# Kernel optimization log

Measured on AMD Instinct MI355X. Metric: run time of the kernel, lower is better.

The kernel has to match this reference:

```python
import jax, jax.numpy as jnp
import numpy as np

N_USER = 50000
N_ITEM = 100000
N_NODES = N_USER + N_ITEM  # 150000
EMB = 64
N_LAYERS = 3
NNZ = 2400000
BATCH = 4096
EPS = 1e-12  # F.normalize eps


def setup_inputs() -> dict:
    key = jax.random.key(0)
    ks = jax.random.split(key, 12)
    return {
        "users": jax.random.randint(ks[0], (BATCH,), 0, N_USER, dtype=jnp.int32),
        "pos_items": jax.random.randint(ks[1], (BATCH,), 0, N_ITEM, dtype=jnp.int32),
        "neg_items": jax.random.randint(ks[2], (BATCH,), 0, N_ITEM, dtype=jnp.int32),
        "adj_row": jax.random.randint(ks[3], (NNZ,), 0, N_NODES, dtype=jnp.int32),
        "adj_col": jax.random.randint(ks[4], (NNZ,), 0, N_NODES, dtype=jnp.int32),
        "adj_val": jax.random.uniform(ks[5], (NNZ,), dtype=jnp.float32),
        "user_emb": jax.random.normal(ks[6], (N_USER, EMB), dtype=jnp.float32) * 0.1,
        "item_emb": jax.random.normal(ks[7], (N_ITEM, EMB), dtype=jnp.float32) * 0.1,
        "W_gc": jax.random.normal(ks[8], (N_LAYERS, EMB, EMB), dtype=jnp.float32) * 0.1,
        "b_gc": jax.random.normal(ks[9], (N_LAYERS, 1, EMB), dtype=jnp.float32) * 0.1,
        "W_bi": jax.random.normal(ks[10], (N_LAYERS, EMB, EMB), dtype=jnp.float32) * 0.1,
        "b_bi": jax.random.normal(ks[11], (N_LAYERS, 1, EMB), dtype=jnp.float32) * 0.1,
    }


def reference(users, pos_items, neg_items, adj_row, adj_col, adj_val,
              user_emb, item_emb, W_gc, b_gc, W_bi, b_bi):
    # ego embeddings: concat user/item tables -> [N_NODES, EMB]
    ego = jnp.concatenate([user_emb, item_emb], axis=0)
    all_embs = [ego]
    for k in range(N_LAYERS):
        # sparse A_hat @ ego via gather + segment-sum over edges
        msgs = adj_val[:, None] * ego[adj_col]            # [NNZ, EMB]
        side = jax.ops.segment_sum(msgs, adj_row, num_segments=N_NODES)
        sum_emb = side @ W_gc[k] + b_gc[k]                # [N, EMB]
        bi_emb = (ego * side) @ W_bi[k] + b_bi[k]         # [N, EMB]
        ego = jax.nn.leaky_relu(sum_emb + bi_emb, negative_slope=0.2)
        # mess_dropout = 0 (eval mode) -> identity
        nrm = jnp.linalg.norm(ego, axis=1, keepdims=True)
        all_embs.append(ego / jnp.maximum(nrm, EPS))
    all_embs = jnp.concatenate(all_embs, axis=1)          # [N, EMB*(L+1)]
    u_g = all_embs[:N_USER]
    i_g = all_embs[N_USER:]
    return (u_g[users], i_g[pos_items], i_g[neg_items])
```

## Files before the change

### kernel.cpp

```cpp
#include <hip/hip_runtime.h>

typedef short bf16x8 __attribute__((ext_vector_type(8)));
typedef float f32x4  __attribute__((ext_vector_type(4)));

#define N_USER 50000
#define N_ITEM 100000
#define N_NODES 150000
#define EMB 64
#define NNZ 2400000
#define BATCH 4096
#define NSAMP (3 * BATCH)
#define NB 256
#define RPB 587
#define BS_GRID 256
#define EPB (NNZ / BS_GRID)
#define CAP 10304

__device__ __forceinline__ unsigned int bf16_rne(float x) {
    unsigned int u = __float_as_uint(x);
    return (u + 0x7fffu + ((u >> 16) & 1u)) >> 16;
}
__device__ __forceinline__ float bflo(unsigned int u) { return __uint_as_float(u << 16); }
__device__ __forceinline__ float bfhi(unsigned int u) { return __uint_as_float(u & 0xffff0000u); }

__device__ __forceinline__ void fma8(float v, const uint4& x, float* acc) {
    acc[0] = fmaf(v, bflo(x.x), acc[0]); acc[1] = fmaf(v, bfhi(x.x), acc[1]);
    acc[2] = fmaf(v, bflo(x.y), acc[2]); acc[3] = fmaf(v, bfhi(x.y), acc[3]);
    acc[4] = fmaf(v, bflo(x.z), acc[4]); acc[5] = fmaf(v, bfhi(x.z), acc[5]);
    acc[6] = fmaf(v, bflo(x.w), acc[6]); acc[7] = fmaf(v, bfhi(x.w), acc[7]);
}
__device__ __forceinline__ uint4 pack8(const float* f) {
    return make_uint4((bf16_rne(f[1]) << 16) | bf16_rne(f[0]),
                      (bf16_rne(f[3]) << 16) | bf16_rne(f[2]),
                      (bf16_rne(f[5]) << 16) | bf16_rne(f[4]),
                      (bf16_rne(f[7]) << 16) | bf16_rne(f[6]));
}
__device__ __forceinline__ uint2 cvt2(const float4& v) {
    return make_uint2((bf16_rne(v.y) << 16) | bf16_rne(v.x),
                      (bf16_rne(v.w) << 16) | bf16_rne(v.z));
}

#define SEG_A (N_NODES * 4)
#define SEG_B (NSAMP * 16)
#define SEG_C (3 * 8192)
#define SEG_D 192
#define INIT_TOT (SEG_A + SEG_B + SEG_C + SEG_D + NSAMP)
#define INIT_BLOCKS ((INIT_TOT + 1023) / 1024)
__global__ __launch_bounds__(1024) void binit(const float4* __restrict__ ue4,
                                              const float4* __restrict__ ie4,
                                              const int* __restrict__ users,
                                              const int* __restrict__ pos,
                                              const int* __restrict__ neg,
                                              uint2* __restrict__ ego_bf,
                                              float* __restrict__ out,
                                              int* __restrict__ samp,
                                              const float* __restrict__ Wgc,
                                              const float* __restrict__ Wbi,
                                              const float* __restrict__ bgc,
                                              const float* __restrict__ bbi,
                                              ushort* __restrict__ wbf,
                                              float* __restrict__ biasf) {
    int idx = blockIdx.x * 1024 + threadIdx.x;
    if (idx >= INIT_TOT) return;
    if (idx < SEG_A) {
        const int NU4 = N_USER * 16;
        int b4 = idx * 4;
        float4 a, b, c, d;
        if (b4 < NU4) { a = ue4[b4]; b = ue4[b4 + 1]; c = ue4[b4 + 2]; d = ue4[b4 + 3]; }
        else { int j = b4 - NU4; a = ie4[j]; b = ie4[j + 1]; c = ie4[j + 2]; d = ie4[j + 3]; }
        uint2 o0 = cvt2(a), o1 = cvt2(b), o2 = cvt2(c), o3 = cvt2(d);
        uint4* e4 = (uint4*)ego_bf;
        e4[idx * 2]     = make_uint4(o0.x, o0.y, o1.x, o1.y);
        e4[idx * 2 + 1] = make_uint4(o2.x, o2.y, o3.x, o3.y);
    } else if (idx < SEG_A + SEG_B) {
        int tt = idx - SEG_A;
        int r = tt >> 4, dq = tt & 15;
        int seg = r >> 12, bi = r & (BATCH - 1);
        int node = (seg == 0) ? users[bi] : N_USER + ((seg == 1) ? pos[bi] : neg[bi]);
        float4 v = (node < N_USER) ? ue4[node * 16 + dq] : ie4[(node - N_USER) * 16 + dq];
        ((float4*)out)[(size_t)r * 64 + dq] = v;
    } else if (idx < SEG_A + SEG_B + SEG_C) {
        int tt = idx - SEG_A - SEG_B;
        int l = tt >> 13, rem = tt & 8191;
        int k = rem >> 6, n = rem & 63;
        float w = (k < 64) ? Wgc[l * 4096 + k * 64 + n] : Wbi[l * 4096 + (k - 64) * 64 + n];
        wbf[l * 8704 + n * 136 + k] = (ushort)bf16_rne(w);
    } else if (idx < SEG_A + SEG_B + SEG_C + SEG_D) {
        int tt = idx - SEG_A - SEG_B - SEG_C;
        biasf[tt] = bgc[tt] + bbi[tt];
    } else {
        int tt = idx - SEG_A - SEG_B - SEG_C - SEG_D;
        int seg = tt >> 12, bi = tt & (BATCH - 1);
        samp[tt] = (seg == 0) ? users[bi] : N_USER + ((seg == 1) ? pos[bi] : neg[bi]);
    }
}

__global__ __launch_bounds__(1024) void bin_scatter(const int* __restrict__ rows,
                                                    const int* __restrict__ cols,
                                                    const float* __restrict__ vals,
                                                    int* __restrict__ gcur,
                                                    int2* __restrict__ tmp_cv) {
    __shared__ int2 sorted[EPB];
    __shared__ int hist[NB];
    __shared__ int excl[NB];
    __shared__ int cur[NB];
    __shared__ int gb[NB];
    const int t = threadIdx.x, blk = blockIdx.x;
    if (t < NB) { hist[t] = 0; cur[t] = 0; }
    __syncthreads();
    const int e0 = blk * EPB;
    for (int i = t; i < EPB; i += 1024) atomicAdd(&hist[rows[e0 + i] / RPB], 1);
    __syncthreads();
    if (t < NB) gb[t] = atomicAdd(&gcur[t], hist[t]);
    if (t < NB) excl[t] = hist[t];
    for (int off = 1; off < NB; off <<= 1) {
        __syncthreads();
        int add = (t < NB && t >= off) ? excl[t - off] : 0;
        __syncthreads();
        if (t < NB) excl[t] += add;
    }
    __syncthreads();
    for (int i = t; i < EPB; i += 1024) {
        int e = e0 + i;
        int r = rows[e];
        int b = r / RPB;
        int slot = atomicAdd(&cur[b], 1);
        unsigned vv = (__float_as_uint(vals[e]) & ~1023u) | (unsigned)(r - b * RPB);
        sorted[excl[b] - hist[b] + slot] = make_int2(cols[e], (int)vv);
    }
    __syncthreads();
    const int w = t >> 6, lane = t & 63;
    for (int b = w; b < NB; b += 16) {
        int lo = excl[b] - hist[b];
        int n = hist[b];
        int2* dst = tmp_cv + (size_t)b * CAP + gb[b];
        for (int k = lane; k < n; k += 64) dst[k] = sorted[lo + k];
    }
}

__global__ __launch_bounds__(1024) void csr_from_bins(const int* __restrict__ gcur,
                                                      const int2* __restrict__ tmp_cv,
                                                      int2* __restrict__ ecv,
                                                      int2* __restrict__ row_se) {
    __shared__ int rcnt[RPB];
    __shared__ int sc[1024];
    const int b = blockIdx.x;
    const int row0 = b * RPB;
    const int t = threadIdx.x;
    const int beg = b * CAP;
    const int cnt = gcur[b];

    if (t < RPB) rcnt[t] = 0;
    __syncthreads();
    for (int i = t; i < cnt; i += 1024) atomicAdd(&rcnt[tmp_cv[beg + i].y & 1023], 1);
    __syncthreads();

    int v = (t < RPB) ? rcnt[t] : 0;
    sc[t] = v;
    for (int off = 1; off < 1024; off <<= 1) {
        __syncthreads();
        int add = (t >= off) ? sc[t - off] : 0;
        __syncthreads();
        sc[t] += add;
    }
    __syncthreads();
    int ex = sc[t] - v;

    int lim = N_NODES - row0;
    if (lim > RPB) lim = RPB;
    if (t < lim) row_se[row0 + t] = make_int2(beg + ex, beg + ex + v);
    if (t < RPB) rcnt[t] = ex;
    __syncthreads();
    for (int i = beg + t; i < beg + cnt; i += 1024) {
        int2 rec = tmp_cv[i];
        int r10 = rec.y & 1023;
        int dst = beg + atomicAdd(&rcnt[r10], 1);
        ecv[dst] = make_int2(rec.x, rec.y & ~1023);
    }
}

__global__ __launch_bounds__(256) void spmm_gemm(const int2* __restrict__ row_se,
                                                 const int2* __restrict__ ecv,
                                                 const uint4* __restrict__ ego_bf,
                                                 const ushort* __restrict__ wbf,
                                                 const float* __restrict__ biasf,
                                                 ushort* __restrict__ ego_out,
                                                 float* __restrict__ inv_norm,
                                                 float* __restrict__ out,
                                                 const int* __restrict__ node_list,
                                                 int n_rows, int out_mode, int col0,
                                                 const ushort* __restrict__ g_ego,
                                                 const float* __restrict__ g_inv,
                                                 const int* __restrict__ g_samp,
                                                 int g_col0) {
    const int t = threadIdx.x;
    const int spmmBlocks = (n_rows + 31) >> 5;
    if ((int)blockIdx.x >= spmmBlocks) {
        int i = (blockIdx.x - spmmBlocks) * 256 + t;
        int r = i >> 6, d = i & 63;
        int node = g_samp[r];
        float v = __uint_as_float(((unsigned int)g_ego[(size_t)node * 64 + d]) << 16) * g_inv[node];
        out[(size_t)r * 256 + g_col0 + d] = v;
        return;
    }

    __shared__ ushort As[32][136];

    const int d8 = t & 7;
    const int rl = t >> 3;
    const int r = blockIdx.x * 32 + rl;
    const bool valid = (r < n_rows);
    const int node = valid ? (node_list ? node_list[r] : r) : 0;
    int s0 = 0, s1 = 0;
    if (valid) { int2 se = row_se[node]; s0 = se.x; s1 = se.y; }
    const uint4 selfv = ego_bf[(size_t)node * 8 + d8];
    const int lbase = (t & 63) & 56;

    float acc[8] = {0.f, 0.f, 0.f, 0.f, 0.f, 0.f, 0.f, 0.f};
    int2 m = make_int2(0, 0);
    if (s0 + d8 < s1) m = ecv[s0 + d8];
    for (int e0 = s0; e0 < s1; e0 += 8) {
        int2 mn = make_int2(0, 0);
        if (e0 + 8 + d8 < s1) mn = ecv[e0 + 8 + d8];
#pragma unroll
        for (int j = 0; j < 8; ++j) {
            int   c = __shfl(m.x, lbase + j);
            float v = __int_as_float(__shfl(m.y, lbase + j));
            const uint4 x = ego_bf[(size_t)c * 8 + d8];
            fma8(v, x, acc);
        }
        m = mn;
    }
    float cs[8] = { bflo(selfv.x) * acc[0], bfhi(selfv.x) * acc[1],
                    bflo(selfv.y) * acc[2], bfhi(selfv.y) * acc[3],
                    bflo(selfv.z) * acc[4], bfhi(selfv.z) * acc[5],
                    bflo(selfv.w) * acc[6], bfhi(selfv.w) * acc[7] };
    *(uint4*)&As[rl][d8 * 8]      = pack8(acc);
    *(uint4*)&As[rl][64 + d8 * 8] = pack8(cs);
    __syncthreads();

    const int wv = t >> 6;
    if (wv >= 2) return;
    const int lane = t & 63;
    const int l15 = lane & 15, quad = lane >> 4;
    const bf16x8* wt8 = (const bf16x8*)wbf;
    const int arow = wv * 16 + l15;

    f32x4 C[4] = {{0,0,0,0}, {0,0,0,0}, {0,0,0,0}, {0,0,0,0}};
#pragma unroll
    for (int ks = 0; ks < 4; ++ks) {
        bf16x8 afr = *(const bf16x8*)&As[arow][(ks * 4 + quad) * 8];
        bf16x8 b0 = wt8[(0 * 16 + l15) * 17 + ks * 4 + quad];
        bf16x8 b1 = wt8[(1 * 16 + l15) * 17 + ks * 4 + quad];
        bf16x8 b2 = wt8[(2 * 16 + l15) * 17 + ks * 4 + quad];
        bf16x8 b3 = wt8[(3 * 16 + l15) * 17 + ks * 4 + quad];
        C[0] = __builtin_amdgcn_mfma_f32_16x16x32_bf16(afr, b0, C[0], 0, 0, 0);
        C[1] = __builtin_amdgcn_mfma_f32_16x16x32_bf16(afr, b1, C[1], 0, 0, 0);
        C[2] = __builtin_amdgcn_mfma_f32_16x16x32_bf16(afr, b2, C[2], 0, 0, 0);
        C[3] = __builtin_amdgcn_mfma_f32_16x16x32_bf16(afr, b3, C[3], 0, 0, 0);
    }

    float bias[4];
#pragma unroll
    for (int nt = 0; nt < 4; ++nt) bias[nt] = biasf[nt * 16 + l15];

    float x[4][4];
    float ss[4] = {0.f, 0.f, 0.f, 0.f};
#pragma unroll
    for (int nt = 0; nt < 4; ++nt)
#pragma unroll
        for (int rg = 0; rg < 4; ++rg) {
            float v = C[nt][rg] + bias[nt];
            v = (v >= 0.f) ? v : 0.2f * v;
            x[nt][rg] = v;
            ss[rg] = fmaf(v, v, ss[rg]);
        }
#pragma unroll
    for (int rg = 0; rg < 4; ++rg) {
        ss[rg] += __shfl_xor(ss[rg], 1);
        ss[rg] += __shfl_xor(ss[rg], 2);
        ss[rg] += __shfl_xor(ss[rg], 4);
        ss[rg] += __shfl_xor(ss[rg], 8);
    }
#pragma unroll
    for (int rg = 0; rg < 4; ++rg) {
        int row = blockIdx.x * 32 + wv * 16 + quad * 4 + rg;
        if (row >= n_rows) continue;
        float invr = 1.0f / fmaxf(sqrtf(ss[rg]), 1e-12f);
        if (out_mode) {
#pragma unroll
            for (int nt = 0; nt < 4; ++nt)
                out[(size_t)row * 256 + col0 + nt * 16 + l15] = x[nt][rg] * invr;
        } else {
#pragma unroll
            for (int nt = 0; nt < 4; ++nt)
                ego_out[(size_t)row * 64 + nt * 16 + l15] = (ushort)bf16_rne(x[nt][rg]);
            if (l15 == 0) inv_norm[row] = invr;
        }
    }
}

extern "C" void kernel_launch(void* const* d_in, const int* in_sizes, int n_in,
                              void* d_out, int out_size, void* d_ws, size_t ws_size,
                              hipStream_t stream) {
    const int* users = (const int*)d_in[0];
    const int* pos   = (const int*)d_in[1];
    const int* neg   = (const int*)d_in[2];
    const int* arow  = (const int*)d_in[3];
    const int* acol  = (const int*)d_in[4];
    const float* aval = (const float*)d_in[5];
    const float* ue   = (const float*)d_in[6];
    const float* ie   = (const float*)d_in[7];
    const float* Wgc  = (const float*)d_in[8];
    const float* bgc  = (const float*)d_in[9];
    const float* Wbi  = (const float*)d_in[10];
    const float* bbi  = (const float*)d_in[11];
    float* out = (float*)d_out;

    char* ws = (char*)d_ws;
    size_t o = 0;
    ushort* ego_a   = (ushort*)(ws + o); o += 19200000;
    ushort* ego_b   = (ushort*)(ws + o); o += 19200000;
    int2*   ecv     = (int2*)  (ws + o); o += (size_t)NB * CAP * 8;
    int2*   tmp_cv  = (int2*)  (ws + o); o += (size_t)NB * CAP * 8;
    int*    gcur    = (int*)   (ws + o); o += 1024;
    int2*   row_se  = (int2*)  (ws + o); o += 1200128;
    float*  inv_a     = (float*)(ws + o); o += 600064;
    float*  inv_b     = (float*)(ws + o); o += 600064;
    int*    samp      = (int*) (ws + o); o += 49152;
    ushort* wbf       = (ushort*)(ws + o); o += 52224;
    float*  biasf     = (float*)(ws + o); o += 768;

    const int gatherBlocks = (NSAMP * EMB) / 256;
    const int spmmN = (N_NODES + 31) / 32;
    const int spmmS = NSAMP / 32;

    hipMemsetAsync(gcur, 0, NB * 4, stream);
    binit<<<INIT_BLOCKS, 1024, 0, stream>>>(
        (const float4*)ue, (const float4*)ie,
        users, pos, neg, (uint2*)ego_a, out, samp,
        Wgc, Wbi, bgc, bbi, wbf, biasf);
    bin_scatter<<<BS_GRID, 1024, 0, stream>>>(arow, acol, aval, gcur, tmp_cv);
    csr_from_bins<<<NB, 1024, 0, stream>>>(gcur, tmp_cv, ecv, row_se);

    spmm_gemm<<<spmmN, 256, 0, stream>>>(
        row_se, ecv, (const uint4*)ego_a, wbf, biasf,
        ego_b, inv_b, out, nullptr, N_NODES, 0, 0,
        nullptr, nullptr, nullptr, 0);

    spmm_gemm<<<spmmN + gatherBlocks, 256, 0, stream>>>(
        row_se, ecv, (const uint4*)ego_b, wbf + 8704, biasf + 64,
        ego_a, inv_a, out, nullptr, N_NODES, 0, 0,
        ego_b, inv_b, samp, 64);

    spmm_gemm<<<spmmS + gatherBlocks, 256, 0, stream>>>(
        row_se, ecv, (const uint4*)ego_a, wbf + 2 * 8704, biasf + 128,
        nullptr, nullptr, out, samp, NSAMP, 1, 192,
        ego_a, inv_a, samp, 128);
}
```

Baseline: 295.5 us.

## Sort rows by degree for SpMM load balance and batch gathers

Adds a per-row degree histogram and a permutation kernel that reorders rows by edge count, so each 32-row SpMM block handles rows of similar length and wave divergence drops. The SpMM reads segment bounds through the permutation and scatters outputs to the original node index. Also issues all 8 neighbor gathers before the FMAs to raise memory-level parallelism, folds the gcur memset into binit, and raises the bin_scatter grid size. This costs an extra kernel launch, scattered output writes, and more registers per thread.

After: 305.6 us. 3.4% more time.

```diff
diff --git a/kernel.cpp b/kernel.cpp
--- a/kernel.cpp
+++ b/kernel.cpp
@@ -12,7 +12,7 @@
 #define NSAMP (3 * BATCH)
 #define NB 256
 #define RPB 587
-#define BS_GRID 256
+#define BS_GRID 500
 #define EPB (NNZ / BS_GRID)
 #define CAP 10304
 
@@ -44,7 +44,8 @@
 #define SEG_B (NSAMP * 16)
 #define SEG_C (3 * 8192)
 #define SEG_D 192
-#define INIT_TOT (SEG_A + SEG_B + SEG_C + SEG_D + NSAMP)
+#define SEG_E 512
+#define INIT_TOT (SEG_A + SEG_B + SEG_C + SEG_D + SEG_E + NSAMP)
 #define INIT_BLOCKS ((INIT_TOT + 1023) / 1024)
 __global__ __launch_bounds__(1024) void binit(const float4* __restrict__ ue4,
                                               const float4* __restrict__ ie4,
@@ -59,7 +60,8 @@
                                               const float* __restrict__ bgc,
                                               const float* __restrict__ bbi,
                                               ushort* __restrict__ wbf,
-                                              float* __restrict__ biasf) {
+                                              float* __restrict__ biasf,
+                                              int* __restrict__ gcur) {
     int idx = blockIdx.x * 1024 + threadIdx.x;
     if (idx >= INIT_TOT) return;
     if (idx < SEG_A) {
@@ -88,8 +90,10 @@
     } else if (idx < SEG_A + SEG_B + SEG_C + SEG_D) {
         int tt = idx - SEG_A - SEG_B - SEG_C;
         biasf[tt] = bgc[tt] + bbi[tt];
+    } else if (idx < SEG_A + SEG_B + SEG_C + SEG_D + SEG_E) {
+        gcur[idx - SEG_A - SEG_B - SEG_C - SEG_D] = 0;
     } else {
-        int tt = idx - SEG_A - SEG_B - SEG_C - SEG_D;
+        int tt = idx - SEG_A - SEG_B - SEG_C - SEG_D - SEG_E;
         int seg = tt >> 12, bi = tt & (BATCH - 1);
         samp[tt] = (seg == 0) ? users[bi] : N_USER + ((seg == 1) ? pos[bi] : neg[bi]);
     }
@@ -141,9 +145,11 @@
 __global__ __launch_bounds__(1024) void csr_from_bins(const int* __restrict__ gcur,
                                                       const int2* __restrict__ tmp_cv,
                                                       int2* __restrict__ ecv,
-                                                      int2* __restrict__ row_se) {
+                                                      int2* __restrict__ row_se,
+                                                      int* __restrict__ pcnt) {
     __shared__ int rcnt[RPB];
     __shared__ int sc[1024];
+    __shared__ int phist[128];
     const int b = blockIdx.x;
     const int row0 = b * RPB;
     const int t = threadIdx.x;
@@ -151,6 +157,7 @@
     const int cnt = gcur[b];
 
     if (t < RPB) rcnt[t] = 0;
+    if (t < 128) phist[t] = 0;
     __syncthreads();
     for (int i = t; i < cnt; i += 1024) atomicAdd(&rcnt[tmp_cv[beg + i].y & 1023], 1);
     __syncthreads();
@@ -168,9 +175,13 @@
 
     int lim = N_NODES - row0;
     if (lim > RPB) lim = RPB;
-    if (t < lim) row_se[row0 + t] = make_int2(beg + ex, beg + ex + v);
+    if (t < lim) {
+        row_se[row0 + t] = make_int2(beg + ex, beg + ex + v);
+        atomicAdd(&phist[min(v, 127)], 1);
+    }
     if (t < RPB) rcnt[t] = ex;
     __syncthreads();
+    if (t < 128 && phist[t]) atomicAdd(&pcnt[t], phist[t]);
     for (int i = beg + t; i < beg + cnt; i += 1024) {
         int2 rec = tmp_cv[i];
         int r10 = rec.y & 1023;
@@ -179,7 +190,44 @@
     }
 }
 
-__global__ __launch_bounds__(256) void spmm_gemm(const int2* __restrict__ row_se,
+__global__ __launch_bounds__(1024) void permk(const int2* __restrict__ row_se,
+                                              const int* __restrict__ pcnt,
+                                              int* __restrict__ pcur,
+                                              int* __restrict__ perm,
+                                              int2* __restrict__ row_sep) {
+    __shared__ int hist[128], lbase[128], lcur[128], psrc[128], pre[128];
+    const int b = blockIdx.x;
+    const int row0 = b * RPB;
+    const int t = threadIdx.x;
+    if (t < 128) { hist[t] = 0; lcur[t] = 0; psrc[t] = pcnt[t]; }
+    __syncthreads();
+    int lim = N_NODES - row0;
+    if (lim > RPB) lim = RPB;
+    int2 se = make_int2(0, 0);
+    int cls = 0;
+    if (t < lim) {
+        se = row_se[row0 + t];
+        cls = min(se.y - se.x, 127);
+        atomicAdd(&hist[cls], 1);
+    }
+    __syncthreads();
+    if (t < 128) {
+        if (hist[t]) lbase[t] = atomicAdd(&pcur[t], hist[t]);
+        int s = 0;
+        for (int c = t + 1; c < 128; ++c) s += psrc[c];
+        pre[t] = s;
+    }
+    __syncthreads();
+    if (t < lim) {
+        int slot = atomicAdd(&lcur[cls], 1);
+        int dst = pre[cls] + lbase[cls] + slot;
+        perm[dst] = row0 + t;
+        row_sep[dst] = se;
+    }
+}
+
+__global__ __launch_bounds__(256) void spmm_gemm(const int2* __restrict__ se_r,
+                                                 const int2* __restrict__ se_node,
                                                  const int2* __restrict__ ecv,
                                                  const uint4* __restrict__ ego_bf,
                                                  const ushort* __restrict__ wbf,
@@ -205,14 +253,19 @@
     }
 
     __shared__ ushort As[32][136];
+    __shared__ int nds[32];
 
     const int d8 = t & 7;
     const int rl = t >> 3;
     const int r = blockIdx.x * 32 + rl;
     const bool valid = (r < n_rows);
     const int node = valid ? (node_list ? node_list[r] : r) : 0;
+    if (d8 == 0) nds[rl] = node;
     int s0 = 0, s1 = 0;
-    if (valid) { int2 se = row_se[node]; s0 = se.x; s1 = se.y; }
+    if (valid) {
+        int2 se = se_r ? se_r[r] : se_node[node];
+        s0 = se.x; s1 = se.y;
+    }
     const uint4 selfv = ego_bf[(size_t)node * 8 + d8];
     const int lbase = (t & 63) & 56;
 
@@ -222,13 +275,18 @@
     for (int e0 = s0; e0 < s1; e0 += 8) {
         int2 mn = make_int2(0, 0);
         if (e0 + 8 + d8 < s1) mn = ecv[e0 + 8 + d8];
+        int   cc[8];
+        float vv[8];
 #pragma unroll
         for (int j = 0; j < 8; ++j) {
-            int   c = __shfl(m.x, lbase + j);
-            float v = __int_as_float(__shfl(m.y, lbase + j));
-            const uint4 x = ego_bf[(size_t)c * 8 + d8];
-            fma8(v, x, acc);
+            cc[j] = __shfl(m.x, lbase + j);
+            vv[j] = __int_as_float(__shfl(m.y, lbase + j));
         }
+        uint4 x[8];
+#pragma unroll
+        for (int j = 0; j < 8; ++j) x[j] = ego_bf[(size_t)cc[j] * 8 + d8];
+#pragma unroll
+        for (int j = 0; j < 8; ++j) fma8(vv[j], x[j], acc);
         m = mn;
     }
     float cs[8] = { bflo(selfv.x) * acc[0], bfhi(selfv.x) * acc[1],
@@ -284,18 +342,20 @@
     }
 #pragma unroll
     for (int rg = 0; rg < 4; ++rg) {
-        int row = blockIdx.x * 32 + wv * 16 + quad * 4 + rg;
-        if (row >= n_rows) continue;
+        int lrow = wv * 16 + quad * 4 + rg;
+        int grow = blockIdx.x * 32 + lrow;
+        if (grow >= n_rows) continue;
         float invr = 1.0f / fmaxf(sqrtf(ss[rg]), 1e-12f);
         if (out_mode) {
 #pragma unroll
             for (int nt = 0; nt < 4; ++nt)
-                out[(size_t)row * 256 + col0 + nt * 16 + l15] = x[nt][rg] * invr;
+                out[(size_t)grow * 256 + col0 + nt * 16 + l15] = x[nt][rg] * invr;
         } else {
+            int nd = nds[lrow];
 #pragma unroll
             for (int nt = 0; nt < 4; ++nt)
-                ego_out[(size_t)row * 64 + nt * 16 + l15] = (ushort)bf16_rne(x[nt][rg]);
-            if (l15 == 0) inv_norm[row] = invr;
+                ego_out[(size_t)nd * 64 + nt * 16 + l15] = (ushort)bf16_rne(x[nt][rg]);
+            if (l15 == 0) inv_norm[nd] = invr;
         }
     }
 }
@@ -323,8 +383,12 @@
     ushort* ego_b   = (ushort*)(ws + o); o += 19200000;
     int2*   ecv     = (int2*)  (ws + o); o += (size_t)NB * CAP * 8;
     int2*   tmp_cv  = (int2*)  (ws + o); o += (size_t)NB * CAP * 8;
-    int*    gcur    = (int*)   (ws + o); o += 1024;
+    int*    gcur    = (int*)   (ws + o); o += 2048;
+    int*    pcnt    = gcur + 256;
+    int*    pcur    = gcur + 384;
     int2*   row_se  = (int2*)  (ws + o); o += 1200128;
+    int2*   row_sep = (int2*)  (ws + o); o += 1200128;
+    int*    perm    = (int*)   (ws + o); o += 600064;
     float*  inv_a     = (float*)(ws + o); o += 600064;
     float*  inv_b     = (float*)(ws + o); o += 600064;
     int*    samp      = (int*) (ws + o); o += 49152;
@@ -335,26 +399,26 @@
     const int spmmN = (N_NODES + 31) / 32;
     const int spmmS = NSAMP / 32;
 
-    hipMemsetAsync(gcur, 0, NB * 4, stream);
     binit<<<INIT_BLOCKS, 1024, 0, stream>>>(
         (const float4*)ue, (const float4*)ie,
         users, pos, neg, (uint2*)ego_a, out, samp,
-        Wgc, Wbi, bgc, bbi, wbf, biasf);
+        Wgc, Wbi, bgc, bbi, wbf, biasf, gcur);
     bin_scatter<<<BS_GRID, 1024, 0, stream>>>(arow, acol, aval, gcur, tmp_cv);
-    csr_from_bins<<<NB, 1024, 0, stream>>>(gcur, tmp_cv, ecv, row_se);
+    csr_from_bins<<<NB, 1024, 0, stream>>>(gcur, tmp_cv, ecv, row_se, pcnt);
+    permk<<<NB, 1024, 0, stream>>>(row_se, pcnt, pcur, perm, row_sep);
 
     spmm_gemm<<<spmmN, 256, 0, stream>>>(
-        row_se, ecv, (const uint4*)ego_a, wbf, biasf,
-        ego_b, inv_b, out, nullptr, N_NODES, 0, 0,
+        row_sep, nullptr, ecv, (const uint4*)ego_a, wbf, biasf,
+        ego_b, inv_b, out, perm, N_NODES, 0, 0,
         nullptr, nullptr, nullptr, 0);
 
     spmm_gemm<<<spmmN + gatherBlocks, 256, 0, stream>>>(
-        row_se, ecv, (const uint4*)ego_b, wbf + 8704, biasf + 64,
-        ego_a, inv_a, out, nullptr, N_NODES, 0, 0,
+        row_sep, nullptr, ecv, (const uint4*)ego_b, wbf + 8704, biasf + 64,
+        ego_a, inv_a, out, perm, N_NODES, 0, 0,
         ego_b, inv_b, samp, 64);
 
     spmm_gemm<<<spmmS + gatherBlocks, 256, 0, stream>>>(
-        row_se, ecv, (const uint4*)ego_a, wbf + 2 * 8704, biasf + 128,
+        nullptr, row_se, ecv, (const uint4*)ego_a, wbf + 2 * 8704, biasf + 128,
         nullptr, nullptr, out, samp, NSAMP, 1, 192,
         ego_a, inv_a, samp, 128);
 }
```

## Merge bin scatter with init kernel and precompute per-row counts globally

Applied to the files above, without the earlier changes.

Fuses the edge bin-scatter and the embedding/weight init into one launch, with the first blocks doing the scatter and the rest doing init. The scatter blocks also build per-row edge counts with global atomics, so csr_from_bins no longer re-reads tmp_cv to histogram rows. The scatter grid grows from 256 to 500 blocks, which shrinks the per-block shared memory buffer. In exchange it adds global atomics that contend on row counters, a larger memset, and init blocks now carry the scatter kernel's shared memory allocation.

Result: slower. 375.8 us (+27.2%).

```diff
diff --git a/kernel.cpp b/kernel.cpp
--- a/kernel.cpp
+++ b/kernel.cpp
@@ -12,7 +12,7 @@
 #define NSAMP (3 * BATCH)
 #define NB 256
 #define RPB 587
-#define BS_GRID 256
+#define BS_GRID 500
 #define EPB (NNZ / BS_GRID)
 #define CAP 10304
 
@@ -46,21 +46,71 @@
 #define SEG_D 192
 #define INIT_TOT (SEG_A + SEG_B + SEG_C + SEG_D + NSAMP)
 #define INIT_BLOCKS ((INIT_TOT + 1023) / 1024)
-__global__ __launch_bounds__(1024) void binit(const float4* __restrict__ ue4,
-                                              const float4* __restrict__ ie4,
-                                              const int* __restrict__ users,
-                                              const int* __restrict__ pos,
-                                              const int* __restrict__ neg,
-                                              uint2* __restrict__ ego_bf,
-                                              float* __restrict__ out,
-                                              int* __restrict__ samp,
-                                              const float* __restrict__ Wgc,
-                                              const float* __restrict__ Wbi,
-                                              const float* __restrict__ bgc,
-                                              const float* __restrict__ bbi,
-                                              ushort* __restrict__ wbf,
-                                              float* __restrict__ biasf) {
-    int idx = blockIdx.x * 1024 + threadIdx.x;
+__global__ __launch_bounds__(1024) void scat_init(const int* __restrict__ rows,
+                                                  const int* __restrict__ cols,
+                                                  const float* __restrict__ vals,
+                                                  int* __restrict__ gcur,
+                                                  int* __restrict__ rcnt_g,
+                                                  int2* __restrict__ tmp_cv,
+                                                  const float4* __restrict__ ue4,
+                                                  const float4* __restrict__ ie4,
+                                                  const int* __restrict__ users,
+                                                  const int* __restrict__ pos,
+                                                  const int* __restrict__ neg,
+                                                  uint2* __restrict__ ego_bf,
+                                                  float* __restrict__ out,
+                                                  int* __restrict__ samp,
+                                                  const float* __restrict__ Wgc,
+                                                  const float* __restrict__ Wbi,
+                                                  const float* __restrict__ bgc,
+                                                  const float* __restrict__ bbi,
+                                                  ushort* __restrict__ wbf,
+                                                  float* __restrict__ biasf) {
+    __shared__ int2 sorted[EPB];
+    __shared__ int hist[NB];
+    __shared__ int excl[NB];
+    __shared__ int cur[NB];
+    __shared__ int gb[NB];
+    const int t = threadIdx.x;
+    if (blockIdx.x < BS_GRID) {
+        const int blk = blockIdx.x;
+        if (t < NB) { hist[t] = 0; cur[t] = 0; }
+        __syncthreads();
+        const int e0 = blk * EPB;
+        for (int i = t; i < EPB; i += 1024) {
+            int r = rows[e0 + i];
+            atomicAdd(&hist[r / RPB], 1);
+            atomicAdd(&rcnt_g[r], 1);
+        }
+        __syncthreads();
+        if (t < NB) gb[t] = atomicAdd(&gcur[t], hist[t]);
+        if (t < NB) excl[t] = hist[t];
+        for (int off = 1; off < NB; off <<= 1) {
+            __syncthreads();
+            int add = (t < NB && t >= off) ? excl[t - off] : 0;
+            __syncthreads();
+            if (t < NB) excl[t] += add;
+        }
+        __syncthreads();
+        for (int i = t; i < EPB; i += 1024) {
+            int e = e0 + i;
+            int r = rows[e];
+            int b = r / RPB;
+            int slot = atomicAdd(&cur[b], 1);
+            unsigned vv = (__float_as_uint(vals[e]) & ~1023u) | (unsigned)(r - b * RPB);
+            sorted[excl[b] - hist[b] + slot] = make_int2(cols[e], (int)vv);
+        }
+        __syncthreads();
+        const int w = t >> 6, lane = t & 63;
+        for (int b = w; b < NB; b += 16) {
+            int lo = excl[b] - hist[b];
+            int n = hist[b];
+            int2* dst = tmp_cv + (size_t)b * CAP + gb[b];
+            for (int k = lane; k < n; k += 64) dst[k] = sorted[lo + k];
+        }
+        return;
+    }
+    int idx = (blockIdx.x - BS_GRID) * 1024 + t;
     if (idx >= INIT_TOT) return;
     if (idx < SEG_A) {
         const int NU4 = N_USER * 16;
@@ -95,54 +145,12 @@
     }
 }
 
-__global__ __launch_bounds__(1024) void bin_scatter(const int* __restrict__ rows,
-                                                    const int* __restrict__ cols,
-                                                    const float* __restrict__ vals,
-                                                    int* __restrict__ gcur,
-                                                    int2* __restrict__ tmp_cv) {
-    __shared__ int2 sorted[EPB];
-    __shared__ int hist[NB];
-    __shared__ int excl[NB];
-    __shared__ int cur[NB];
-    __shared__ int gb[NB];
-    const int t = threadIdx.x, blk = blockIdx.x;
-    if (t < NB) { hist[t] = 0; cur[t] = 0; }
-    __syncthreads();
-    const int e0 = blk * EPB;
-    for (int i = t; i < EPB; i += 1024) atomicAdd(&hist[rows[e0 + i] / RPB], 1);
-    __syncthreads();
-    if (t < NB) gb[t] = atomicAdd(&gcur[t], hist[t]);
-    if (t < NB) excl[t] = hist[t];
-    for (int off = 1; off < NB; off <<= 1) {
-        __syncthreads();
-        int add = (t < NB && t >= off) ? excl[t - off] : 0;
-        __syncthreads();
-        if (t < NB) excl[t] += add;
-    }
-    __syncthreads();
-    for (int i = t; i < EPB; i += 1024) {
-        int e = e0 + i;
-        int r = rows[e];
-        int b = r / RPB;
-        int slot = atomicAdd(&cur[b], 1);
-        unsigned vv = (__float_as_uint(vals[e]) & ~1023u) | (unsigned)(r - b * RPB);
-        sorted[excl[b] - hist[b] + slot] = make_int2(cols[e], (int)vv);
-    }
-    __syncthreads();
-    const int w = t >> 6, lane = t & 63;
-    for (int b = w; b < NB; b += 16) {
-        int lo = excl[b] - hist[b];
-        int n = hist[b];
-        int2* dst = tmp_cv + (size_t)b * CAP + gb[b];
-        for (int k = lane; k < n; k += 64) dst[k] = sorted[lo + k];
-    }
-}
-
 __global__ __launch_bounds__(1024) void csr_from_bins(const int* __restrict__ gcur,
+                                                      const int* __restrict__ rcnt_g,
                                                       const int2* __restrict__ tmp_cv,
                                                       int2* __restrict__ ecv,
                                                       int2* __restrict__ row_se) {
-    __shared__ int rcnt[RPB];
+    __shared__ int rcur[RPB];
     __shared__ int sc[1024];
     const int b = blockIdx.x;
     const int row0 = b * RPB;
@@ -150,12 +158,7 @@
     const int beg = b * CAP;
     const int cnt = gcur[b];
 
-    if (t < RPB) rcnt[t] = 0;
-    __syncthreads();
-    for (int i = t; i < cnt; i += 1024) atomicAdd(&rcnt[tmp_cv[beg + i].y & 1023], 1);
-    __syncthreads();
-
-    int v = (t < RPB) ? rcnt[t] : 0;
+    int v = (t < RPB) ? rcnt_g[row0 + t] : 0;
     sc[t] = v;
     for (int off = 1; off < 1024; off <<= 1) {
         __syncthreads();
@@ -169,12 +172,12 @@
     int lim = N_NODES - row0;
     if (lim > RPB) lim = RPB;
     if (t < lim) row_se[row0 + t] = make_int2(beg + ex, beg + ex + v);
-    if (t < RPB) rcnt[t] = ex;
+    if (t < RPB) rcur[t] = ex;
     __syncthreads();
     for (int i = beg + t; i < beg + cnt; i += 1024) {
         int2 rec = tmp_cv[i];
         int r10 = rec.y & 1023;
-        int dst = beg + atomicAdd(&rcnt[r10], 1);
+        int dst = beg + atomicAdd(&rcur[r10], 1);
         ecv[dst] = make_int2(rec.x, rec.y & ~1023);
     }
 }
@@ -324,6 +327,7 @@
     int2*   ecv     = (int2*)  (ws + o); o += (size_t)NB * CAP * 8;
     int2*   tmp_cv  = (int2*)  (ws + o); o += (size_t)NB * CAP * 8;
     int*    gcur    = (int*)   (ws + o); o += 1024;
+    int*    rcnt_g  = (int*)   (ws + o); o += 150272 * 4;
     int2*   row_se  = (int2*)  (ws + o); o += 1200128;
     float*  inv_a     = (float*)(ws + o); o += 600064;
     float*  inv_b     = (float*)(ws + o); o += 600064;
@@ -335,13 +339,13 @@
     const int spmmN = (N_NODES + 31) / 32;
     const int spmmS = NSAMP / 32;
 
-    hipMemsetAsync(gcur, 0, NB * 4, stream);
-    binit<<<INIT_BLOCKS, 1024, 0, stream>>>(
+    hipMemsetAsync(gcur, 0, 1024 + 150272 * 4, stream);
+    scat_init<<<BS_GRID + INIT_BLOCKS, 1024, 0, stream>>>(
+        arow, acol, aval, gcur, rcnt_g, tmp_cv,
         (const float4*)ue, (const float4*)ie,
         users, pos, neg, (uint2*)ego_a, out, samp,
         Wgc, Wbi, bgc, bbi, wbf, biasf);
-    bin_scatter<<<BS_GRID, 1024, 0, stream>>>(arow, acol, aval, gcur, tmp_cv);
-    csr_from_bins<<<NB, 1024, 0, stream>>>(gcur, tmp_cv, ecv, row_se);
+    csr_from_bins<<<NB, 1024, 0, stream>>>(gcur, rcnt_g, tmp_cv, ecv, row_se);
 
     spmm_gemm<<<spmmN, 256, 0, stream>>>(
         row_se, ecv, (const uint4*)ego_a, wbf, biasf,
```
